# Kernel optimization log

Hardware: AMD Instinct MI355X
Metric: run time of the kernel (lower is better)

Reference implementation:

```python
import jax, jax.numpy as jnp
import numpy as np

MARGIN = 0.3
NEG_INF = jnp.float32(-1e30)


def setup_inputs() -> dict:
    key = jax.random.key(0)
    k1, k2 = jax.random.split(key)
    features = jax.random.normal(k1, (8192, 128), dtype=jnp.float32)
    labels = jax.random.randint(k2, (8192,), 0, 512)
    return {"features": features, "labels": labels}


def reference(features, labels):
    n = features.shape[0]
    # pairwise Euclidean distance, clamped like the torch code
    x2 = jnp.sum(features * features, axis=1, keepdims=True)          # [N,1]
    d2 = x2 + x2.T - 2.0 * (features @ features.T)                    # [N,N]
    dist = jnp.sqrt(jnp.clip(d2, 1e-8))

    same = labels[None, :] == labels[:, None]                          # [N,N]
    eye = jnp.eye(n, dtype=bool)
    pos_mask = same & ~eye                                             # positives, self excluded
    neg_mask = ~same

    # soft mining: softmax-weighted positive distance (weights ~ softmax(d))
    pos_logits = jnp.where(pos_mask, dist, NEG_INF)
    pw = jax.nn.softmax(pos_logits, axis=1)
    wp = jnp.sum(pw * jnp.where(pos_mask, dist, 0.0), axis=1)          # [N]

    # softmax-weighted negative distance (weights ~ softmax(-d))
    neg_logits = jnp.where(neg_mask, -dist, NEG_INF)
    nw = jax.nn.softmax(neg_logits, axis=1)
    wn = jnp.sum(nw * jnp.where(neg_mask, dist, 0.0), axis=1)          # [N]

    # soft margin: softplus(diff + margin)
    loss = jax.nn.softplus(wp - wn + MARGIN)

    # rows without any positive or any negative are skipped in the original
    valid = pos_mask.any(axis=1) & neg_mask.any(axis=1)
    loss = jnp.where(valid, loss, 0.0)
    denom = jnp.maximum(jnp.sum(valid.astype(jnp.float32)), 1.0)
    return jnp.sum(loss) / denom
```

## Files before the change

kernel.cpp:

```cpp
#include <hip/hip_runtime.h>
#include <hip/hip_bf16.h>


typedef __bf16 bf16x8 __attribute__((ext_vector_type(8)));
typedef float f32x4 __attribute__((ext_vector_type(4)));

#define NROWS 8192
#define DIM 128
#define JTILE 64
#define LDS_STRIDE 136
#define NLABELS 512
#define GCAP 64
#define MARGIN_F 0.3f
#define AK1F 2.04027892f
#define EPS_T 2.08137e-8f
#define C2F (-43.2808512f)
#define LN2F 0.69314718f

__global__ __launch_bounds__(256) void prep_kernel(const float* __restrict__ F,
                                                   const int* __restrict__ labels,
                                                   __hip_bfloat16* __restrict__ Fb,
                                                   float* __restrict__ x2,
                                                   int* __restrict__ gcnt,
                                                   int* __restrict__ gslot) {
    const int tid = threadIdx.x;
    const int wave = tid >> 6, lane = tid & 63;
    const int row = blockIdx.x * 4 + wave;
    float2 f = ((const float2*)(F + (size_t)row * DIM))[lane];
    f.x *= AK1F; f.y *= AK1F;
    ((__hip_bfloat162*)(Fb + (size_t)row * DIM))[lane] = __float22bfloat162_rn(f);
    float ss = f.x * f.x + f.y * f.y;
#pragma unroll
    for (int m = 32; m > 0; m >>= 1) ss += __shfl_xor(ss, m, 64);
    if (lane == 0) {
        x2[row] = ss;
        const int lab = labels[row];
        int pos = atomicAdd(&gcnt[lab], 1);
        if (pos < GCAP) gslot[lab * GCAP + pos] = row;
    }
}

template<bool DIAG>
__device__ __forceinline__ void tile_body(const __hip_bfloat16* __restrict__ sB,
                                          const float* __restrict__ sX2h,
                                          const bf16x8 (&a)[2][4],
                                          const float (&x2ih)[2][4],
                                          float (&nl)[2][4], float (&ns)[2][4],
                                          int lm, int quad, int ibase, int jbase) {
#pragma unroll
    for (int jt = 0; jt < 4; ++jt) {
        const int jl = jt * 16 + lm;
        const __hip_bfloat16* bp = sB + jl * LDS_STRIDE + quad * 8;
        bf16x8 b[4];
#pragma unroll
        for (int kc = 0; kc < 4; ++kc) b[kc] = *(const bf16x8*)(bp + kc * 32);
        const float xjh = sX2h[jl];
#pragma unroll
        for (int g = 0; g < 2; ++g) {
            f32x4 acc;
#pragma unroll
            for (int r = 0; r < 4; ++r) acc[r] = x2ih[g][r] + xjh;
#pragma unroll
            for (int kc = 0; kc < 4; ++kc)
                acc = __builtin_amdgcn_mfma_f32_16x16x32_bf16(a[g][kc], b[kc], acc, 0, 0, 0);
            const int djg = jbase + jl - (ibase + g * 16 + quad * 4);
#pragma unroll
            for (int r = 0; r < 4; ++r) {
                float d2h = fmaxf(-acc[r], EPS_T);
                float t = __builtin_amdgcn_sqrtf(d2h);
                float ne = __builtin_amdgcn_exp2f(-t);
                if (DIAG) ne = (djg == r) ? 0.f : ne;
                nl[g][r] += ne;
                ns[g][r] = fmaf(ne, t, ns[g][r]);
            }
        }
    }
}

__global__ __launch_bounds__(256)
__attribute__((amdgpu_waves_per_eu(4, 4)))
void pairs_kernel(
        const __hip_bfloat16* __restrict__ Fb,
        const float* __restrict__ x2,
        const int* __restrict__ gcnt,
        const int* __restrict__ gslot,
        float2* __restrict__ partial,
        float4* __restrict__ corr,
        int jspan) {
    __shared__ __hip_bfloat16 sB[JTILE * LDS_STRIDE];
    __shared__ float sX2h[JTILE];

    const int tid = threadIdx.x;
    const int wave = tid >> 6;
    const int lane = tid & 63;
    const int quad = lane >> 4;
    const int lm = lane & 15;
    const int ibase = blockIdx.x * 128 + wave * 32;

    bf16x8 a[2][4];
#pragma unroll
    for (int g = 0; g < 2; ++g)
#pragma unroll
        for (int kc = 0; kc < 4; ++kc)
            a[g][kc] = *(const bf16x8*)(Fb + (size_t)(ibase + g * 16 + lm) * DIM
                                        + kc * 32 + quad * 8);

    float x2ih[2][4];
#pragma unroll
    for (int g = 0; g < 2; ++g)
#pragma unroll
        for (int r = 0; r < 4; ++r)
            x2ih[g][r] = -0.5f * x2[ibase + g * 16 + quad * 4 + r];

    float nl[2][4] = {}, ns[2][4] = {};

    const int j0 = blockIdx.y * jspan;
    const int jiters = jspan >> 6;
    const int djb0 = 2 * (int)blockIdx.x - (int)blockIdx.y * jiters;

    for (int jb = 0; jb < jiters; ++jb) {
        const int jbase = j0 + jb * JTILE;
        __syncthreads();
#pragma unroll
        for (int s = 0; s < 4; ++s) {
            int c = tid + s * 256;
            int jr = c >> 4, ck = c & 15;
            *(bf16x8*)(sB + jr * LDS_STRIDE + ck * 8) =
                *(const bf16x8*)(Fb + (size_t)(jbase + jr) * DIM + ck * 8);
        }
        if (tid < JTILE) sX2h[tid] = -0.5f * x2[jbase + tid];
        __syncthreads();

        if ((unsigned)(jb - djb0) <= 1u)
            tile_body<true >(sB, sX2h, a, x2ih, nl, ns, lm, quad, ibase, jbase);
        else
            tile_body<false>(sB, sX2h, a, x2ih, nl, ns, lm, quad, ibase, jbase);
    }

#pragma unroll
    for (int m = 1; m < 16; m <<= 1) {
#pragma unroll
        for (int g = 0; g < 2; ++g)
#pragma unroll
            for (int r = 0; r < 4; ++r) {
                nl[g][r] += __shfl_xor(nl[g][r], m, 64);
                ns[g][r] += __shfl_xor(ns[g][r], m, 64);
            }
    }
    if (lm == 0) {
#pragma unroll
        for (int g = 0; g < 2; ++g)
#pragma unroll
            for (int r = 0; r < 4; ++r)
                partial[(size_t)blockIdx.y * NROWS + ibase + g * 16 + quad * 4 + r] =
                    make_float2(nl[g][r], ns[g][r]);
    }

    if (blockIdx.y > 1) return;
    __syncthreads();
    float* sAcc = (float*)sB;
    float* plA = sAcc;
    float* psA = sAcc + GCAP;
    float* nlA = sAcc + 2 * GCAP;
    float* nsA = sAcc + 3 * GCAP;
    const int cid = (int)blockIdx.x * 2 + (int)blockIdx.y;

    for (int li = 0; li < NLABELS / 128; ++li) {
        const int L = cid * (NLABELS / 128) + li;
        const int cnt = gcnt[L];
        const int gsz = cnt < GCAP ? cnt : GCAP;
        if (tid < GCAP) { plA[tid] = 0.f; psA[tid] = 0.f; nlA[tid] = 0.f; nsA[tid] = 0.f; }
        __syncthreads();
        const int npair = gsz * gsz;
        for (int p = tid; p < npair; p += 256) {
            const int aI = p / gsz, bI = p - aI * gsz;
            if (aI != bI) {
                const int ia = gslot[L * GCAP + aI];
                const int ib = gslot[L * GCAP + bI];
                const bf16x8* pa = (const bf16x8*)(Fb + (size_t)ia * DIM);
                const bf16x8* pb = (const bf16x8*)(Fb + (size_t)ib * DIM);
                float dot = 0.f;
#pragma unroll 4
                for (int u = 0; u < 16; ++u) {
                    bf16x8 va = pa[u], vb = pb[u];
#pragma unroll
                    for (int e = 0; e < 8; ++e)
                        dot = fmaf((float)va[e], (float)vb[e], dot);
                }
                float d2h = fmaxf(0.5f * (x2[ia] + x2[ib]) - dot, EPS_T);
                float t = __builtin_amdgcn_sqrtf(d2h);
                float ne = __builtin_amdgcn_exp2f(-t);
                float pe = __builtin_amdgcn_exp2f(t + C2F);
                unsafeAtomicAdd(&nlA[aI], ne);
                unsafeAtomicAdd(&nsA[aI], ne * t);
                unsafeAtomicAdd(&plA[aI], pe);
                unsafeAtomicAdd(&psA[aI], pe * t);
            }
        }
        __syncthreads();
        if (tid < gsz)
            corr[gslot[L * GCAP + tid]] =
                make_float4(plA[tid], psA[tid], -nlA[tid], -nsA[tid]);
        __syncthreads();
    }
}

__global__ __launch_bounds__(256) void finalize_kernel(const float2* __restrict__ partial,
                                                       const float4* __restrict__ corr,
                                                       float* __restrict__ gstat,
                                                       float* __restrict__ out,
                                                       int jsplit) {
    const int row = blockIdx.x * 256 + threadIdx.x;
    float4 c = corr[row];
    float nl = c.z, ns = c.w;
    for (int s = 0; s < jsplit; ++s) {
        float2 p = partial[(size_t)s * NROWS + row];
        nl += p.x; ns += p.y;
    }
    float sum = 0.f, cnt = 0.f;
    if (c.x > 0.f && nl > 0.f) {
        float x = fmaf(LN2F, c.y / c.x - ns / nl, MARGIN_F);
        sum = fmaxf(x, 0.f) + log1pf(__expf(-fabsf(x)));
        cnt = 1.f;
    }
#pragma unroll
    for (int m = 32; m > 0; m >>= 1) {
        sum += __shfl_xor(sum, m, 64);
        cnt += __shfl_xor(cnt, m, 64);
    }
    __shared__ float sS[4], sC[4];
    const int wave = threadIdx.x >> 6, lane = threadIdx.x & 63;
    if (lane == 0) { sS[wave] = sum; sC[wave] = cnt; }
    __syncthreads();
    if (threadIdx.x == 0) {
        unsafeAtomicAdd(&gstat[0], sS[0] + sS[1] + sS[2] + sS[3]);
        unsafeAtomicAdd(&gstat[1], sC[0] + sC[1] + sC[2] + sC[3]);
        __threadfence();
        unsigned t = atomicAdd((unsigned int*)(gstat + 2), 1u);
        if (t == (unsigned)(gridDim.x - 1)) {
            float s2 = unsafeAtomicAdd(&gstat[0], 0.f);
            float c2 = unsafeAtomicAdd(&gstat[1], 0.f);
            out[0] = s2 / fmaxf(c2, 1.f);
        }
    }
}

extern "C" void kernel_launch(void* const* d_in, const int* in_sizes, int n_in,
                              void* d_out, int out_size, void* d_ws, size_t ws_size,
                              hipStream_t stream) {
    const float* F = (const float*)d_in[0];
    const int* labels = (const int*)d_in[1];
    float* out = (float*)d_out;

    char* ws = (char*)d_ws;
    __hip_bfloat16* Fb = (__hip_bfloat16*)ws;
    size_t off = (size_t)NROWS * DIM * 2;
    float* x2 = (float*)(ws + off);   off += (size_t)NROWS * 4;
    float4* corr = (float4*)(ws + off); off += (size_t)NROWS * 16;
    int* gcnt = (int*)(ws + off);     off += (size_t)NLABELS * 4;
    float* gstat = (float*)(ws + off); off += 16;
    int* gslot = (int*)(ws + off);    off += (size_t)NLABELS * GCAP * 4;

    int jsplit = 16;
    while (jsplit > 2 && off + (size_t)jsplit * NROWS * 8 > ws_size) jsplit >>= 1;
    float2* partial = (float2*)(ws + off);

    hipMemsetAsync(gcnt, 0, (size_t)NLABELS * 4 + 16, stream);
    prep_kernel<<<NROWS / 4, 256, 0, stream>>>(F, labels, Fb, x2, gcnt, gslot);
    pairs_kernel<<<dim3(NROWS / 128, jsplit), 256, 0, stream>>>(
        Fb, x2, gcnt, gslot, partial, corr, NROWS / jsplit);
    finalize_kernel<<<NROWS / 256, 256, 0, stream>>>(partial, corr, gstat, out, jsplit);
}
```

Measured before the change: 126.1 us.

## Halve rows per block, move label-group work to block prologue across more blocks

Each wave now handles 16 rows instead of 32, which halves the A-fragment registers, and the grid doubles to NROWS/64 blocks. The per-label positive-pair correction now runs at the start of blocks with y<4, one label per block, instead of being looped at the tail of y<=1 blocks. This spreads that serial tail across 512 blocks, and launch bounds are changed to (256,4). In exchange, each B tile is reused over fewer rows, so LDS loads per MFMA double, and jsplit now has a minimum of 4.

New measurement: 115.8 us. -8.2%, faster.

```diff
diff --git a/kernel.cpp b/kernel.cpp
--- a/kernel.cpp
+++ b/kernel.cpp
@@ -43,43 +43,37 @@
 template<bool DIAG>
 __device__ __forceinline__ void tile_body(const __hip_bfloat16* __restrict__ sB,
                                           const float* __restrict__ sX2h,
-                                          const bf16x8 (&a)[2][4],
-                                          const float (&x2ih)[2][4],
-                                          float (&nl)[2][4], float (&ns)[2][4],
-                                          int lm, int quad, int ibase, int jbase) {
+                                          const bf16x8 (&a)[4],
+                                          const float (&x2ih)[4],
+                                          float (&nl4)[4], float (&ns4)[4],
+                                          int lm, int quad, int ig0, int jbase) {
 #pragma unroll
     for (int jt = 0; jt < 4; ++jt) {
         const int jl = jt * 16 + lm;
         const __hip_bfloat16* bp = sB + jl * LDS_STRIDE + quad * 8;
-        bf16x8 b[4];
-#pragma unroll
-        for (int kc = 0; kc < 4; ++kc) b[kc] = *(const bf16x8*)(bp + kc * 32);
         const float xjh = sX2h[jl];
-#pragma unroll
-        for (int g = 0; g < 2; ++g) {
-            f32x4 acc;
-#pragma unroll
-            for (int r = 0; r < 4; ++r) acc[r] = x2ih[g][r] + xjh;
-#pragma unroll
-            for (int kc = 0; kc < 4; ++kc)
-                acc = __builtin_amdgcn_mfma_f32_16x16x32_bf16(a[g][kc], b[kc], acc, 0, 0, 0);
-            const int djg = jbase + jl - (ibase + g * 16 + quad * 4);
-#pragma unroll
-            for (int r = 0; r < 4; ++r) {
-                float d2h = fmaxf(-acc[r], EPS_T);
-                float t = __builtin_amdgcn_sqrtf(d2h);
-                float ne = __builtin_amdgcn_exp2f(-t);
-                if (DIAG) ne = (djg == r) ? 0.f : ne;
-                nl[g][r] += ne;
-                ns[g][r] = fmaf(ne, t, ns[g][r]);
-            }
-        }
-    }
-}
-
-__global__ __launch_bounds__(256)
-__attribute__((amdgpu_waves_per_eu(4, 4)))
-void pairs_kernel(
+        f32x4 acc;
+#pragma unroll
+        for (int r = 0; r < 4; ++r) acc[r] = x2ih[r] + xjh;
+#pragma unroll
+        for (int kc = 0; kc < 4; ++kc) {
+            bf16x8 b = *(const bf16x8*)(bp + kc * 32);
+            acc = __builtin_amdgcn_mfma_f32_16x16x32_bf16(a[kc], b, acc, 0, 0, 0);
+        }
+        const int dj = jbase + jl - ig0;
+#pragma unroll
+        for (int r = 0; r < 4; ++r) {
+            float d2h = fmaxf(-acc[r], EPS_T);
+            float t = __builtin_amdgcn_sqrtf(d2h);
+            float ne = __builtin_amdgcn_exp2f(-t);
+            if (DIAG) ne = (dj == r) ? 0.f : ne;
+            nl4[r] += ne;
+            ns4[r] = fmaf(ne, t, ns4[r]);
+        }
+    }
+}
+
+__global__ __launch_bounds__(256, 4) void pairs_kernel(
         const __hip_bfloat16* __restrict__ Fb,
         const float* __restrict__ x2,
         const int* __restrict__ gcnt,
@@ -91,32 +85,73 @@
     __shared__ float sX2h[JTILE];
 
     const int tid = threadIdx.x;
+
+    if (blockIdx.y < 4) {
+        const int L = (int)blockIdx.y * 128 + (int)blockIdx.x;
+        float* sAcc = (float*)sB;
+        float* plA = sAcc;
+        float* psA = sAcc + GCAP;
+        float* nlA = sAcc + 2 * GCAP;
+        float* nsA = sAcc + 3 * GCAP;
+        const int cnt = gcnt[L];
+        const int gsz = cnt < GCAP ? cnt : GCAP;
+        if (gsz > 0) {
+            if (tid < GCAP) { plA[tid] = 0.f; psA[tid] = 0.f; nlA[tid] = 0.f; nsA[tid] = 0.f; }
+            __syncthreads();
+            const int npair = gsz * gsz;
+            for (int p = tid; p < npair; p += 256) {
+                const int aI = p / gsz, bI = p - aI * gsz;
+                if (aI != bI) {
+                    const int ia = gslot[L * GCAP + aI];
+                    const int ib = gslot[L * GCAP + bI];
+                    const bf16x8* pa = (const bf16x8*)(Fb + (size_t)ia * DIM);
+                    const bf16x8* pb = (const bf16x8*)(Fb + (size_t)ib * DIM);
+                    float dot = 0.f;
+#pragma unroll 4
+                    for (int u = 0; u < 16; ++u) {
+                        bf16x8 va = pa[u], vb = pb[u];
+#pragma unroll
+                        for (int e = 0; e < 8; ++e)
+                            dot = fmaf((float)va[e], (float)vb[e], dot);
+                    }
+                    float d2h = fmaxf(0.5f * (x2[ia] + x2[ib]) - dot, EPS_T);
+                    float t = __builtin_amdgcn_sqrtf(d2h);
+                    float ne = __builtin_amdgcn_exp2f(-t);
+                    float pe = __builtin_amdgcn_exp2f(t + C2F);
+                    unsafeAtomicAdd(&nlA[aI], ne);
+                    unsafeAtomicAdd(&nsA[aI], ne * t);
+                    unsafeAtomicAdd(&plA[aI], pe);
+                    unsafeAtomicAdd(&psA[aI], pe * t);
+                }
+            }
+            __syncthreads();
+            if (tid < gsz)
+                corr[gslot[L * GCAP + tid]] =
+                    make_float4(plA[tid], psA[tid], -nlA[tid], -nsA[tid]);
+        }
+    }
+
     const int wave = tid >> 6;
     const int lane = tid & 63;
     const int quad = lane >> 4;
     const int lm = lane & 15;
-    const int ibase = blockIdx.x * 128 + wave * 32;
-
-    bf16x8 a[2][4];
-#pragma unroll
-    for (int g = 0; g < 2; ++g)
-#pragma unroll
-        for (int kc = 0; kc < 4; ++kc)
-            a[g][kc] = *(const bf16x8*)(Fb + (size_t)(ibase + g * 16 + lm) * DIM
-                                        + kc * 32 + quad * 8);
-
-    float x2ih[2][4];
-#pragma unroll
-    for (int g = 0; g < 2; ++g)
-#pragma unroll
-        for (int r = 0; r < 4; ++r)
-            x2ih[g][r] = -0.5f * x2[ibase + g * 16 + quad * 4 + r];
-
-    float nl[2][4] = {}, ns[2][4] = {};
+    const int rbase = blockIdx.x * 64 + wave * 16;
+
+    bf16x8 a[4];
+#pragma unroll
+    for (int kc = 0; kc < 4; ++kc)
+        a[kc] = *(const bf16x8*)(Fb + (size_t)(rbase + lm) * DIM + kc * 32 + quad * 8);
+
+    const int ig0 = rbase + quad * 4;
+    float x2ih[4];
+#pragma unroll
+    for (int r = 0; r < 4; ++r) x2ih[r] = -0.5f * x2[ig0 + r];
+
+    float nl4[4] = {0,0,0,0}, ns4[4] = {0,0,0,0};
 
     const int j0 = blockIdx.y * jspan;
     const int jiters = jspan >> 6;
-    const int djb0 = 2 * (int)blockIdx.x - (int)blockIdx.y * jiters;
+    const int djb = (int)blockIdx.x - (int)blockIdx.y * jiters;
 
     for (int jb = 0; jb < jiters; ++jb) {
         const int jbase = j0 + jb * JTILE;
@@ -131,77 +166,25 @@
         if (tid < JTILE) sX2h[tid] = -0.5f * x2[jbase + tid];
         __syncthreads();
 
-        if ((unsigned)(jb - djb0) <= 1u)
-            tile_body<true >(sB, sX2h, a, x2ih, nl, ns, lm, quad, ibase, jbase);
+        if (jb == djb)
+            tile_body<true >(sB, sX2h, a, x2ih, nl4, ns4, lm, quad, ig0, jbase);
         else
-            tile_body<false>(sB, sX2h, a, x2ih, nl, ns, lm, quad, ibase, jbase);
+            tile_body<false>(sB, sX2h, a, x2ih, nl4, ns4, lm, quad, ig0, jbase);
     }
 
 #pragma unroll
     for (int m = 1; m < 16; m <<= 1) {
 #pragma unroll
-        for (int g = 0; g < 2; ++g)
-#pragma unroll
-            for (int r = 0; r < 4; ++r) {
-                nl[g][r] += __shfl_xor(nl[g][r], m, 64);
-                ns[g][r] += __shfl_xor(ns[g][r], m, 64);
-            }
+        for (int r = 0; r < 4; ++r) {
+            nl4[r] += __shfl_xor(nl4[r], m, 64);
+            ns4[r] += __shfl_xor(ns4[r], m, 64);
+        }
     }
     if (lm == 0) {
 #pragma unroll
-        for (int g = 0; g < 2; ++g)
-#pragma unroll
-            for (int r = 0; r < 4; ++r)
-                partial[(size_t)blockIdx.y * NROWS + ibase + g * 16 + quad * 4 + r] =
-                    make_float2(nl[g][r], ns[g][r]);
-    }
-
-    if (blockIdx.y > 1) return;
-    __syncthreads();
-    float* sAcc = (float*)sB;
-    float* plA = sAcc;
-    float* psA = sAcc + GCAP;
-    float* nlA = sAcc + 2 * GCAP;
-    float* nsA = sAcc + 3 * GCAP;
-    const int cid = (int)blockIdx.x * 2 + (int)blockIdx.y;
-
-    for (int li = 0; li < NLABELS / 128; ++li) {
-        const int L = cid * (NLABELS / 128) + li;
-        const int cnt = gcnt[L];
-        const int gsz = cnt < GCAP ? cnt : GCAP;
-        if (tid < GCAP) { plA[tid] = 0.f; psA[tid] = 0.f; nlA[tid] = 0.f; nsA[tid] = 0.f; }
-        __syncthreads();
-        const int npair = gsz * gsz;
-        for (int p = tid; p < npair; p += 256) {
-            const int aI = p / gsz, bI = p - aI * gsz;
-            if (aI != bI) {
-                const int ia = gslot[L * GCAP + aI];
-                const int ib = gslot[L * GCAP + bI];
-                const bf16x8* pa = (const bf16x8*)(Fb + (size_t)ia * DIM);
-                const bf16x8* pb = (const bf16x8*)(Fb + (size_t)ib * DIM);
-                float dot = 0.f;
-#pragma unroll 4
-                for (int u = 0; u < 16; ++u) {
-                    bf16x8 va = pa[u], vb = pb[u];
-#pragma unroll
-                    for (int e = 0; e < 8; ++e)
-                        dot = fmaf((float)va[e], (float)vb[e], dot);
-                }
-                float d2h = fmaxf(0.5f * (x2[ia] + x2[ib]) - dot, EPS_T);
-                float t = __builtin_amdgcn_sqrtf(d2h);
-                float ne = __builtin_amdgcn_exp2f(-t);
-                float pe = __builtin_amdgcn_exp2f(t + C2F);
-                unsafeAtomicAdd(&nlA[aI], ne);
-                unsafeAtomicAdd(&nsA[aI], ne * t);
-                unsafeAtomicAdd(&plA[aI], pe);
-                unsafeAtomicAdd(&psA[aI], pe * t);
-            }
-        }
-        __syncthreads();
-        if (tid < gsz)
-            corr[gslot[L * GCAP + tid]] =
-                make_float4(plA[tid], psA[tid], -nlA[tid], -nsA[tid]);
-        __syncthreads();
+        for (int r = 0; r < 4; ++r)
+            partial[(size_t)blockIdx.y * NROWS + ig0 + r] =
+                make_float2(nl4[r], ns4[r]);
     }
 }
 
@@ -262,12 +245,12 @@
     int* gslot = (int*)(ws + off);    off += (size_t)NLABELS * GCAP * 4;
 
     int jsplit = 16;
-    while (jsplit > 2 && off + (size_t)jsplit * NROWS * 8 > ws_size) jsplit >>= 1;
+    while (jsplit > 4 && off + (size_t)jsplit * NROWS * 8 > ws_size) jsplit >>= 1;
     float2* partial = (float2*)(ws + off);
 
     hipMemsetAsync(gcnt, 0, (size_t)NLABELS * 4 + 16, stream);
     prep_kernel<<<NROWS / 4, 256, 0, stream>>>(F, labels, Fb, x2, gcnt, gslot);
-    pairs_kernel<<<dim3(NROWS / 128, jsplit), 256, 0, stream>>>(
+    pairs_kernel<<<dim3(NROWS / 64, jsplit), 256, 0, stream>>>(
         Fb, x2, gcnt, gslot, partial, corr, NROWS / jsplit);
     finalize_kernel<<<NROWS / 256, 256, 0, stream>>>(partial, corr, gstat, out, jsplit);
 }
```
